# Optimization experiments

Hardware: AMD Instinct MI355X
Metric: run time of the kernel (lower is better)

The kernel has to match this reference:

```python
import jax, jax.numpy as jnp
import numpy as np

B, T, V = 64, 32, 50257


def setup_inputs() -> dict:
    key = jax.random.key(0)
    k1, k2, k3 = jax.random.split(key, 3)
    logit_rwc = jax.random.normal(k1, (B, T, V), dtype=jnp.float32)
    cap_rwc_label = jax.random.randint(k2, (B, T), 0, V, dtype=jnp.int32)
    # lengths in [1, T] so every sample has at least one valid position
    cap_len_rwc = jax.random.randint(k3, (B,), 1, T + 1, dtype=jnp.int32)
    return {"logit_rwc": logit_rwc, "cap_rwc_label": cap_rwc_label,
            "cap_len_rwc": cap_len_rwc}


def reference(logit_rwc, cap_rwc_label, cap_len_rwc):
    # model_type == 'OFA': keep label ids > 2
    p = jax.nn.softmax(logit_rwc, axis=2)                      # [B,T,V]
    tmask = (jnp.arange(T)[None, :] < cap_len_rwc[:, None]).astype(p.dtype)
    agg = jnp.einsum('btv,bt->bv', p, tmask)                   # masked sum over valid tokens
    sig = jax.nn.sigmoid(agg)                                  # [B,V]
    lmask = (cap_rwc_label > 2).astype(p.dtype)                # [B,T]
    cnt = lmask.sum(axis=1)                                    # >=1 with overwhelming prob
    prob = jnp.take_along_axis(sig, cap_rwc_label, axis=1)     # [B,T]
    loss_cov = ((-jnp.log(prob)) * lmask).sum(axis=1) / cnt
    prob_sm = jnp.take_along_axis(agg, cap_rwc_label, axis=1)  # [B,T]
    loss_rep = (((1.0 - prob_sm) ** 2) * lmask).sum(axis=1) / cnt
    return loss_cov.mean() + loss_rep.mean()
```

## Files before the change

kernel.cpp:

```cpp
#include <hip/hip_runtime.h>

#define BB 64
#define TT 32
#define VV 50257
#define NSEG 8
#define SEGLEN 6284
#define GRID1 2048

__global__ __launch_bounds__(256) void seg_sumexp(
    const float* __restrict__ logits,
    const int*   __restrict__ labels,
    const int*   __restrict__ lens,
    float*       __restrict__ partial,
    float*       __restrict__ numer)
{
    __shared__ int   cum[BB + 1];
    __shared__ float wsum[4];
    const int tid = threadIdx.x;

    if (tid < 64) {
        int inc = lens[tid];
        #pragma unroll
        for (int off = 1; off < 64; off <<= 1) {
            int o = __shfl_up(inc, off);
            if (tid >= off) inc += o;
        }
        cum[tid + 1] = inc;
        if (tid == 0) cum[0] = 0;
    }
    __syncthreads();
    const int total_sids = cum[BB] * NSEG;

    const int sid_lo = (int)(((long long)blockIdx.x * total_sids) / GRID1);
    const int sid_hi = (int)(((long long)(blockIdx.x + 1) * total_sids) / GRID1);

    for (int sid = sid_lo; sid < sid_hi; ++sid) {
        const int r   = sid >> 3;
        const int seg = sid & (NSEG - 1);

        int lo = 0, hi = BB;
        #pragma unroll
        for (int it = 0; it < 6; ++it) {
            const int mid = (lo + hi) >> 1;
            if (cum[mid] <= r) lo = mid; else hi = mid;
        }
        const int b  = lo;
        const int t  = r - cum[b];
        const int bt = b * TT + t;

        const float* row = logits + (size_t)bt * VV;
        const int seg_lo = seg * SEGLEN;
        const int seg_hi = (seg_lo + SEGLEN < VV) ? (seg_lo + SEGLEN) : VV;
        const int n = seg_hi - seg_lo;
        const float* p0 = row + seg_lo;

        int head = (int)(((16u - (unsigned)((uintptr_t)p0 & 15u)) & 15u) >> 2);
        if (head > n) head = n;

        float a0 = 0.f, a1 = 0.f, a2 = 0.f, a3 = 0.f;
        for (int i = tid; i < head; i += 256) a0 += __expf(p0[i]);
        const float4* pv = (const float4*)(p0 + head);
        const int nvec = (n - head) >> 2;
        for (int i = tid; i < nvec; i += 256) {
            float4 x = pv[i];
            a0 += __expf(x.x); a1 += __expf(x.y);
            a2 += __expf(x.z); a3 += __expf(x.w);
        }
        for (int i = head + (nvec << 2) + tid; i < n; i += 256) a0 += __expf(p0[i]);

        float acc = (a0 + a1) + (a2 + a3);
        #pragma unroll
        for (int off = 32; off >= 1; off >>= 1) acc += __shfl_xor(acc, off);
        if ((tid & 63) == 0) wsum[tid >> 6] = acc;
        __syncthreads();
        if (tid == 0)
            partial[bt * NSEG + seg] = (wsum[0] + wsum[1]) + (wsum[2] + wsum[3]);

        if (tid < TT) {
            const int l = labels[b * TT + tid];
            if (l >= seg_lo && l < seg_hi) numer[bt * TT + tid] = __expf(row[l]);
        }
        __syncthreads();
    }
}

__global__ __launch_bounds__(64) void loss_reduce(
    const int*   __restrict__ labels,
    const int*   __restrict__ lens,
    const float* __restrict__ partial,
    const float* __restrict__ numer,
    float*       __restrict__ out)
{
    const int b   = blockIdx.x;
    const int tid = threadIdx.x;
    const int len = lens[b];

    __shared__ float sinv[TT];
    if (tid < len) {
        float s = 0.f;
        #pragma unroll
        for (int seg = 0; seg < NSEG; ++seg)
            s += partial[(b * TT + tid) * NSEG + seg];
        sinv[tid] = 1.0f / s;
    }
    __syncthreads();

    float agg = 0.f;
    if (tid < TT) {
        for (int t = 0; t < len; ++t)
            agg += numer[(b * TT + t) * TT + tid] * sinv[t];
    }

    float cov = 0.f, rep = 0.f, cnt = 0.f;
    if (tid < TT) {
        const int l = labels[b * TT + tid];
        if (l > 2) {
            cov = log1pf(__expf(-agg));
            const float d = 1.0f - agg;
            rep = d * d;
            cnt = 1.0f;
        }
    }
    #pragma unroll
    for (int off = 32; off >= 1; off >>= 1) {
        cov += __shfl_xor(cov, off);
        rep += __shfl_xor(rep, off);
        cnt += __shfl_xor(cnt, off);
    }
    if (tid == 0) atomicAdd(out, (cov + rep) / cnt * (1.0f / BB));
}

extern "C" void kernel_launch(void* const* d_in, const int* in_sizes, int n_in,
                              void* d_out, int out_size, void* d_ws, size_t ws_size,
                              hipStream_t stream) {
    const float* logits = (const float*)d_in[0];
    const int*   labels = (const int*)d_in[1];
    const int*   lens   = (const int*)d_in[2];
    float* out = (float*)d_out;

    float* partial = (float*)d_ws;
    float* numer   = (float*)((char*)d_ws + BB * TT * NSEG * sizeof(float));

    hipMemsetAsync(out, 0, sizeof(float), stream);
    seg_sumexp<<<GRID1, 256, 0, stream>>>(logits, labels, lens, partial, numer);
    loss_reduce<<<BB, 64, 0, stream>>>(labels, lens, partial, numer, out);
}
```

Baseline: 49.17 us.

## Split valid logits evenly across blocks by element range and single-block reduce

Replaces the fixed 8-segments-per-row work split with an exact element-range partition of all valid rows, so each block streams a contiguous, equal-sized slice that spans at most two rows. Per-block partial sums are tagged with their row index and combined by a single-block reduce kernel using shared-memory atomics, which also drops the memset and the global atomic. This is meant to remove load imbalance from segment granularity and to cut one launch. In exchange the final reduction runs on a single block, and the fixed two-entry-per-block layout assumes each slice is shorter than one row.

```diff
diff --git a/kernel.cpp b/kernel.cpp
--- a/kernel.cpp
+++ b/kernel.cpp
@@ -3,15 +3,14 @@
 #define BB 64
 #define TT 32
 #define VV 50257
-#define NSEG 8
-#define SEGLEN 6284
 #define GRID1 2048
 
-__global__ __launch_bounds__(256) void seg_sumexp(
+__global__ __launch_bounds__(256) void stream_sumexp(
     const float* __restrict__ logits,
     const int*   __restrict__ labels,
     const int*   __restrict__ lens,
-    float*       __restrict__ partial,
+    float*       __restrict__ blk_sum,
+    int*         __restrict__ blk_bt,
     float*       __restrict__ numer)
 {
     __shared__ int   cum[BB + 1];
@@ -29,15 +28,14 @@
         if (tid == 0) cum[0] = 0;
     }
     __syncthreads();
-    const int total_sids = cum[BB] * NSEG;
+    const long long E = (long long)cum[BB] * VV;
+    const int e_lo = (int)((E * blockIdx.x) / GRID1);
+    const int e_hi = (int)((E * (blockIdx.x + 1)) / GRID1);
+    const int r0 = e_lo / VV;
+    const int r1 = (e_hi - 1) / VV;
 
-    const int sid_lo = (int)(((long long)blockIdx.x * total_sids) / GRID1);
-    const int sid_hi = (int)(((long long)(blockIdx.x + 1) * total_sids) / GRID1);
-
-    for (int sid = sid_lo; sid < sid_hi; ++sid) {
-        const int r   = sid >> 3;
-        const int seg = sid & (NSEG - 1);
-
+    int c = 0;
+    for (int r = r0; r <= r1; ++r, ++c) {
         int lo = 0, hi = BB;
         #pragma unroll
         for (int it = 0; it < 6; ++it) {
@@ -48,11 +46,13 @@
         const int t  = r - cum[b];
         const int bt = b * TT + t;
 
+        const int rbase = r * VV;
+        const int s_loc = (e_lo > rbase ? e_lo : rbase) - rbase;
+        const int e_loc = ((e_hi < rbase + VV) ? e_hi : rbase + VV) - rbase;
+        const int n = e_loc - s_loc;
+
         const float* row = logits + (size_t)bt * VV;
-        const int seg_lo = seg * SEGLEN;
-        const int seg_hi = (seg_lo + SEGLEN < VV) ? (seg_lo + SEGLEN) : VV;
-        const int n = seg_hi - seg_lo;
-        const float* p0 = row + seg_lo;
+        const float* p0  = row + s_loc;
 
         int head = (int)(((16u - (unsigned)((uintptr_t)p0 & 15u)) & 15u) >> 2);
         if (head > n) head = n;
@@ -66,68 +66,84 @@
             a0 += __expf(x.x); a1 += __expf(x.y);
             a2 += __expf(x.z); a3 += __expf(x.w);
         }
-        for (int i = head + (nvec << 2) + tid; i < n; i += 256) a0 += __expf(p0[i]);
+        for (int k = head + (nvec << 2) + tid; k < n; k += 256) a0 += __expf(p0[k]);
 
         float acc = (a0 + a1) + (a2 + a3);
         #pragma unroll
         for (int off = 32; off >= 1; off >>= 1) acc += __shfl_xor(acc, off);
         if ((tid & 63) == 0) wsum[tid >> 6] = acc;
         __syncthreads();
-        if (tid == 0)
-            partial[bt * NSEG + seg] = (wsum[0] + wsum[1]) + (wsum[2] + wsum[3]);
+        if (tid == 0) {
+            blk_sum[blockIdx.x * 2 + c] = (wsum[0] + wsum[1]) + (wsum[2] + wsum[3]);
+            blk_bt [blockIdx.x * 2 + c] = bt;
+        }
 
         if (tid < TT) {
             const int l = labels[b * TT + tid];
-            if (l >= seg_lo && l < seg_hi) numer[bt * TT + tid] = __expf(row[l]);
+            if (l >= s_loc && l < e_loc) numer[bt * TT + tid] = __expf(row[l]);
         }
         __syncthreads();
     }
+    if (tid == 0 && c < 2) blk_bt[blockIdx.x * 2 + 1] = -1;
 }
 
-__global__ __launch_bounds__(64) void loss_reduce(
+__global__ __launch_bounds__(256) void loss_reduce(
     const int*   __restrict__ labels,
     const int*   __restrict__ lens,
-    const float* __restrict__ partial,
+    const float* __restrict__ blk_sum,
+    const int*   __restrict__ blk_bt,
     const float* __restrict__ numer,
     float*       __restrict__ out)
 {
-    const int b   = blockIdx.x;
+    __shared__ float s_inv[BB * TT];
+    __shared__ float lsum[8];
     const int tid = threadIdx.x;
-    const int len = lens[b];
 
-    __shared__ float sinv[TT];
-    if (tid < len) {
-        float s = 0.f;
-        #pragma unroll
-        for (int seg = 0; seg < NSEG; ++seg)
-            s += partial[(b * TT + tid) * NSEG + seg];
-        sinv[tid] = 1.0f / s;
+    for (int i = tid; i < BB * TT; i += 256) s_inv[i] = 0.f;
+    __syncthreads();
+    for (int i = tid; i < GRID1 * 2; i += 256) {
+        const int bt = blk_bt[i];
+        if (bt >= 0) atomicAdd(&s_inv[bt], blk_sum[i]);
     }
     __syncthreads();
+    for (int i = tid; i < BB * TT; i += 256) s_inv[i] = 1.0f / s_inv[i];
+    __syncthreads();
 
-    float agg = 0.f;
-    if (tid < TT) {
+    const int g  = tid >> 5;
+    const int tp = tid & 31;
+    float loss_local = 0.f;
+
+    for (int rnd = 0; rnd < 8; ++rnd) {
+        const int b   = rnd * 8 + g;
+        const int len = lens[b];
+        float agg = 0.f;
         for (int t = 0; t < len; ++t)
-            agg += numer[(b * TT + t) * TT + tid] * sinv[t];
-    }
+            agg += numer[(b * TT + t) * TT + tp] * s_inv[b * TT + t];
 
-    float cov = 0.f, rep = 0.f, cnt = 0.f;
-    if (tid < TT) {
-        const int l = labels[b * TT + tid];
+        const int l = labels[b * TT + tp];
+        float cov = 0.f, rep = 0.f, cnt = 0.f;
         if (l > 2) {
             cov = log1pf(__expf(-agg));
             const float d = 1.0f - agg;
             rep = d * d;
             cnt = 1.0f;
         }
+        #pragma unroll
+        for (int off = 16; off >= 1; off >>= 1) {
+            cov += __shfl_xor(cov, off);
+            rep += __shfl_xor(rep, off);
+            cnt += __shfl_xor(cnt, off);
+        }
+        if (tp == 0) loss_local += (cov + rep) / cnt;
     }
-    #pragma unroll
-    for (int off = 32; off >= 1; off >>= 1) {
-        cov += __shfl_xor(cov, off);
-        rep += __shfl_xor(rep, off);
-        cnt += __shfl_xor(cnt, off);
+    if (tp == 0) lsum[g] = loss_local;
+    __syncthreads();
+    if (tid == 0) {
+        float tot = 0.f;
+        #pragma unroll
+        for (int q = 0; q < 8; ++q) tot += lsum[q];
+        out[0] = tot * (1.0f / BB);
     }
-    if (tid == 0) atomicAdd(out, (cov + rep) / cnt * (1.0f / BB));
 }
 
 extern "C" void kernel_launch(void* const* d_in, const int* in_sizes, int n_in,
@@ -138,10 +154,10 @@
     const int*   lens   = (const int*)d_in[2];
     float* out = (float*)d_out;
 
-    float* partial = (float*)d_ws;
-    float* numer   = (float*)((char*)d_ws + BB * TT * NSEG * sizeof(float));
+    float* blk_sum = (float*)d_ws;
+    int*   blk_bt  = (int*)((char*)d_ws + GRID1 * 2 * sizeof(float));
+    float* numer   = (float*)((char*)d_ws + 2 * GRID1 * 2 * sizeof(float));
 
-    hipMemsetAsync(out, 0, sizeof(float), stream);
-    seg_sumexp<<<GRID1, 256, 0, stream>>>(logits, labels, lens, partial, numer);
-    loss_reduce<<<BB, 64, 0, stream>>>(labels, lens, partial, numer, out);
+    stream_sumexp<<<GRID1, 256, 0, stream>>>(logits, labels, lens, blk_sum, blk_bt, numer);
+    loss_reduce<<<1, 256, 0, stream>>>(labels, lens, blk_sum, blk_bt, numer, out);
 }
```

Result: slower. 69.21 us (+40.8%).
